# Optimization experiments

Hardware: AMD Instinct MI355X
Metric: run time of the kernel (lower is better)

Reference implementation:

```python
import jax, jax.numpy as jnp
import numpy as np

N = 2048            # number_of_nodes
E = 32768           # random edges (avg degree 16); self-loops added in forward
D_IN = 3            # node attrs: uncertainty, agent_presence, target
D_PAD = 5           # padded feature width (original pads [N,3] -> [N,5] with zeros)
D_H = 3             # GAT hidden / MHA embed / TransformerConv dims
L_GAT = 10          # GAT num_layers


def _seg_softmax(logits, seg, n):
    # numerically-stable softmax over incoming edges of each destination node
    m = jax.ops.segment_max(logits, seg, num_segments=n)
    e = jnp.exp(logits - m[seg])
    s = jax.ops.segment_sum(e, seg, num_segments=n)
    return e / (s[seg] + 1e-16)


def setup_inputs() -> dict:
    key = jax.random.key(0)
    ks = jax.random.split(key, 32)
    def nrm(k, shape, scale=0.3):
        return (jax.random.normal(k, shape) * scale).astype(jnp.float32)
    return {
        "x": jax.random.uniform(ks[0], (N, D_IN), dtype=jnp.float32),
        "edge_index": jax.random.randint(ks[1], (2, E), 0, N, dtype=jnp.int32),
        "mask": jax.random.uniform(ks[2], (N,), dtype=jnp.float32),
        # 10-layer GAT (heads=1): first layer 5->3, rest 3->3
        "gat_W0": nrm(ks[3], (D_PAD, D_H)),
        "gat_W": nrm(ks[4], (L_GAT - 1, D_H, D_H)),
        "gat_att_src": nrm(ks[5], (L_GAT, D_H)),
        "gat_att_dst": nrm(ks[6], (L_GAT, D_H)),
        "gat_bias": nrm(ks[7], (L_GAT, D_H)),
        # MultiheadAttention(embed_dim=3, num_heads=3, head_dim=1)
        "mha_Wq": nrm(ks[8], (D_H, D_H)), "mha_bq": nrm(ks[9], (D_H,)),
        "mha_Wk": nrm(ks[10], (D_H, D_H)), "mha_bk": nrm(ks[11], (D_H,)),
        "mha_Wv": nrm(ks[12], (D_H, D_H)), "mha_bv": nrm(ks[13], (D_H,)),
        "mha_Wo": nrm(ks[14], (D_H, D_H)), "mha_bo": nrm(ks[15], (D_H,)),
        # TransformerConv(3 -> 3, heads=1) with root-weight skip
        "tc_Wq": nrm(ks[16], (D_H, D_H)), "tc_bq": nrm(ks[17], (D_H,)),
        "tc_Wk": nrm(ks[18], (D_H, D_H)), "tc_bk": nrm(ks[19], (D_H,)),
        "tc_Wv": nrm(ks[20], (D_H, D_H)), "tc_bv": nrm(ks[21], (D_H,)),
        "tc_Wskip": nrm(ks[22], (D_H, D_H)), "tc_bskip": nrm(ks[23], (D_H,)),
        # actor MLP (per-node; MLPAggregation with index = arange(N)): 5 -> 16 -> 32 -> 1
        "mlp_W1": nrm(ks[24], (D_PAD, 16)), "mlp_b1": nrm(ks[25], (16,)),
        "mlp_W2": nrm(ks[26], (16, 32)), "mlp_b2": nrm(ks[27], (32,)),
        "mlp_W3": nrm(ks[28], (32, 1)), "mlp_b3": nrm(ks[29], (1,)),
        # critic Linear(1, 1)
        "critic_W": nrm(ks[30], (1, 1)), "critic_b": nrm(ks[31], (1,)),
    }


def reference(x, edge_index, mask, gat_W0, gat_W, gat_att_src, gat_att_dst, gat_bias,
              mha_Wq, mha_bq, mha_Wk, mha_bk, mha_Wv, mha_bv, mha_Wo, mha_bo,
              tc_Wq, tc_bq, tc_Wk, tc_bk, tc_Wv, tc_bv, tc_Wskip, tc_bskip,
              mlp_W1, mlp_b1, mlp_W2, mlp_b2, mlp_W3, mlp_b3, critic_W, critic_b):
    n = x.shape[0]
    # pad node features [N,3] -> [N,5] with zeros, as in original forward
    h = jnp.concatenate([x, jnp.zeros((n, D_PAD - x.shape[1]), x.dtype)], axis=1)
    # add self loops (add_self_loops in original)
    loop = jnp.arange(n, dtype=edge_index.dtype)
    ei = jnp.concatenate([edge_index, jnp.stack([loop, loop])], axis=1)
    src, dst = ei[0], ei[1]
    # ---- 10-layer GAT (heads=1), ReLU between layers, none after last ----
    for l in range(L_GAT):
        W = gat_W0 if l == 0 else gat_W[l - 1]
        hW = h @ W                                   # [N, 3]
        a_s = hW @ gat_att_src[l]                    # [N]
        a_d = hW @ gat_att_dst[l]                    # [N]
        e = jax.nn.leaky_relu(a_s[src] + a_d[dst], negative_slope=0.2)
        alpha = _seg_softmax(e, dst, n)              # per-destination softmax
        h = jax.ops.segment_sum(alpha[:, None] * hW[src], dst, num_segments=n) + gat_bias[l]
        if l < L_GAT - 1:
            h = jax.nn.relu(h)
    gat_x = h                                        # [N, 3]
    # ---- self multihead attention (first call: history == [gat_x]) ----
    q = (gat_x @ mha_Wq + mha_bq).T[:, :, None]      # [H, N, 1]; head_dim = 1
    k = (gat_x @ mha_Wk + mha_bk).T[:, :, None]
    v = (gat_x @ mha_Wv + mha_bv).T[:, :, None]
    scores = jnp.einsum('hnd,hmd->hnm', q, k)        # scale = head_dim**-0.5 = 1
    attn = jax.nn.softmax(scores, axis=-1)
    ctx = jnp.einsum('hnm,hmd->hnd', attn, v)        # [H, N, 1]
    res = ctx[:, :, 0].T @ mha_Wo + mha_bo           # [N, 3]
    # ---- TransformerConv(3 -> 3, heads=1) with root skip ----
    tq = res @ tc_Wq + tc_bq
    tk = res @ tc_Wk + tc_bk
    tv = res @ tc_Wv + tc_bv
    logits = (tq[dst] * tk[src]).sum(-1) / jnp.sqrt(3.0)
    alpha = _seg_softmax(logits, dst, n)
    agg = jax.ops.segment_sum(alpha[:, None] * tv[src], dst, num_segments=n)
    out = agg + res @ tc_Wskip + tc_bskip            # [N, 3]
    # pad again to 5 channels
    out5 = jnp.concatenate([out, jnp.zeros((n, D_PAD - out.shape[1]), out.dtype)], axis=1)
    # ---- actor: per-node MLP (MLPAggregation, index = arange(N) -> identity batching) ----
    h1 = jax.nn.relu(out5 @ mlp_W1 + mlp_b1)
    h2 = jax.nn.relu(h1 @ mlp_W2 + mlp_b2)
    results = h2 @ mlp_W3 + mlp_b3                   # [N, 1]
    new_results = results[:, 0] * mask               # [N]
    value = (results @ critic_W + critic_b).mean()   # scalar
    return new_results, value
```

## Files before the change

### kernel.cpp

```cpp
#include <hip/hip_runtime.h>
#include <cstdint>

#define NN   2048
#define EIN  32768
#define NB   64
#define BT   1024
#define OPB  32
#define ECAP 4096
#define RS3  0.5773502691896258f

#define WS_BAR   0
#define WS_HA    128
#define WS_HB    (WS_HA + 32768)
#define WS_TKA   (WS_HB + 32768)
#define WS_TKB   (WS_TKA + 32768)
#define WS_VPART (WS_TKB + 16384)

static __device__ __forceinline__ uint64_t cload64(const void* p) {
    return __hip_atomic_load((const uint64_t*)p, __ATOMIC_RELAXED, __HIP_MEMORY_SCOPE_AGENT);
}
static __device__ __forceinline__ void cstore64(void* p, uint64_t v) {
    __hip_atomic_store((uint64_t*)p, v, __ATOMIC_RELAXED, __HIP_MEMORY_SCOPE_AGENT);
}
static __device__ __forceinline__ float4 cloadf4(const float4* p) {
    union { float4 f; uint64_t u[2]; } c;
    c.u[0] = cload64(p); c.u[1] = cload64((const char*)p + 8);
    return c.f;
}
static __device__ __forceinline__ void cstoref4(float4* p, float4 v) {
    union { float4 f; uint64_t u[2]; } c; c.f = v;
    cstore64(p, c.u[0]); cstore64((char*)p + 8, c.u[1]);
}
static __device__ __forceinline__ float2 cloadf2(const float2* p) {
    union { float2 f; uint64_t u; } c; c.u = cload64(p); return c.f;
}
static __device__ __forceinline__ void cstoref2(float2* p, float2 v) {
    union { float2 f; uint64_t u; } c; c.f = v; cstore64(p, c.u);
}
static __device__ __forceinline__ float cloadf(const float* p) {
    union { float f; uint32_t u; } c;
    c.u = __hip_atomic_load((const uint32_t*)p, __ATOMIC_RELAXED, __HIP_MEMORY_SCOPE_AGENT);
    return c.f;
}
static __device__ __forceinline__ void cstoref(float* p, float v) {
    union { float f; uint32_t u; } c; c.f = v;
    __hip_atomic_store((uint32_t*)p, c.u, __ATOMIC_RELAXED, __HIP_MEMORY_SCOPE_AGENT);
}

static __device__ __forceinline__ void gbar(int* bar, int target) {
    __syncthreads();
    if (threadIdx.x == 0) {
        __hip_atomic_fetch_add(bar, 1, __ATOMIC_RELAXED, __HIP_MEMORY_SCOPE_AGENT);
        while (__hip_atomic_load(bar, __ATOMIC_RELAXED, __HIP_MEMORY_SCOPE_AGENT) < target)
            __builtin_amdgcn_s_sleep(4);
    }
    __syncthreads();
}

__global__ __launch_bounds__(BT) void k_fused(
    const float* __restrict__ x, const int* __restrict__ ei,
    const float* __restrict__ maskp,
    const float* __restrict__ gW0, const float* __restrict__ gW,
    const float* __restrict__ atts, const float* __restrict__ attd,
    const float* __restrict__ gbias,
    const float* __restrict__ mWq, const float* __restrict__ mbq,
    const float* __restrict__ mWk, const float* __restrict__ mbk,
    const float* __restrict__ mWv, const float* __restrict__ mbv,
    const float* __restrict__ mWo, const float* __restrict__ mbo,
    const float* __restrict__ tWq, const float* __restrict__ tbq,
    const float* __restrict__ tWk, const float* __restrict__ tbk,
    const float* __restrict__ tWv, const float* __restrict__ tbv,
    const float* __restrict__ tWs, const float* __restrict__ tbs,
    const float* __restrict__ W1, const float* __restrict__ b1,
    const float* __restrict__ W2, const float* __restrict__ b2,
    const float* __restrict__ W3, const float* __restrict__ b3,
    const float* __restrict__ cW, const float* __restrict__ cb,
    char* __restrict__ ws, float* __restrict__ outp)
{
    __shared__ float4 hw4[NN];
    __shared__ __align__(16) char pool[49152];
    __shared__ unsigned short srcs[ECAP];
    __shared__ int   offs[OPB + 1];
    __shared__ int   cntL[OPB];
    __shared__ int   curL[OPB];
    __shared__ float adL[OPB];
    __shared__ float4 ownH[OPB], tqL[OPB], skipL[OPB];
    __shared__ float ctxL[3][OPB];
    __shared__ float redf[96];
    __shared__ float resL[OPB];
    __shared__ float Mhd[6];

    int*    bar   = (int*)(ws + WS_BAR);
    float4* ha    = (float4*)(ws + WS_HA);
    float4* hb    = (float4*)(ws + WS_HB);
    float4* tka   = (float4*)(ws + WS_TKA);
    float2* tkb   = (float2*)(ws + WS_TKB);
    float*  vpart = (float*)(ws + WS_VPART);

    const int tid  = threadIdx.x;
    const int bid  = blockIdx.x;
    const int lane = tid & 63;
    const int wid  = tid >> 6;
    const int R0   = bid * OPB;

    if (tid < OPB) cntL[tid] = 1;
    __syncthreads();
    for (int e = tid; e < EIN; e += BT) {
        unsigned rel = (unsigned)(ei[EIN + e] - R0);
        if (rel < OPB) atomicAdd(&cntL[rel], 1);
    }
    __syncthreads();
    if (tid < 64) {
        int c = (tid < OPB) ? cntL[tid] : 0;
        int v = c;
        #pragma unroll
        for (int d = 1; d < 32; d <<= 1) {
            int u = __shfl_up(v, d);
            if (tid >= d) v += u;
        }
        if (tid < OPB) {
            offs[tid + 1] = v;
            curL[tid] = v - c + 1;
            srcs[v - c] = (unsigned short)(R0 + tid);
        }
        if (tid == 0) offs[0] = 0;
    }
    __syncthreads();
    for (int e = tid; e < EIN; e += BT) {
        unsigned rel = (unsigned)(ei[EIN + e] - R0);
        if (rel < OPB) {
            int p = atomicAdd(&curL[rel], 1);
            if (p < ECAP) srcs[p] = (unsigned short)ei[e];
        }
    }
    __syncthreads();

    for (int l = 0; l < 10; ++l) {
        float4* hprev = (l & 1) ? ha : hb;
        float4* hcur  = (l & 1) ? hb : ha;
        const float* W = l ? (gW + (l - 1) * 9) : gW0;
        float w00=W[0],w01=W[1],w02=W[2],w10=W[3],w11=W[4],w12=W[5],w20=W[6],w21=W[7],w22=W[8];
        float s0=atts[3*l],s1=atts[3*l+1],s2=atts[3*l+2];
        float d0=attd[3*l],d1=attd[3*l+1],d2=attd[3*l+2];
        float bb0=gbias[3*l],bb1=gbias[3*l+1],bb2=gbias[3*l+2];
        #pragma unroll
        for (int i = 0; i < 2; ++i) {
            int n = tid + i * BT;
            float hx, hy, hz;
            if (l == 0) { hx = x[3*n]; hy = x[3*n+1]; hz = x[3*n+2]; }
            else { float4 g = cloadf4(&hprev[n]); hx = g.x; hy = g.y; hz = g.z; }
            float p0 = fmaf(hx, w00, fmaf(hy, w10, hz * w20));
            float p1 = fmaf(hx, w01, fmaf(hy, w11, hz * w21));
            float p2 = fmaf(hx, w02, fmaf(hy, w12, hz * w22));
            hw4[n] = make_float4(p0, p1, p2, fmaf(p0, s0, fmaf(p1, s1, p2 * s2)));
            unsigned rel = (unsigned)(n - R0);
            if (rel < OPB) adL[rel] = fmaf(p0, d0, fmaf(p1, d1, p2 * d2));
        }
        __syncthreads();
        {
            int j = tid >> 5, sub = tid & 31;
            int ps = offs[j], pe = offs[j + 1];
            float ad = adL[j];
            float m = -1e30f, se = 0.f, a0 = 0.f, a1 = 0.f, a2 = 0.f;
            for (int p = ps + sub; p < pe; p += 32) {
                float4 hs = hw4[srcs[p]];
                float lg = hs.w + ad;
                lg = (lg > 0.f) ? lg : 0.2f * lg;
                float nm = fmaxf(m, lg);
                float rr = __expf(m - nm);
                float wg = __expf(lg - nm);
                se = se*rr + wg;
                a0 = a0*rr + wg*hs.x;
                a1 = a1*rr + wg*hs.y;
                a2 = a2*rr + wg*hs.z;
                m = nm;
            }
            #pragma unroll
            for (int d = 1; d < 32; d <<= 1) {
                float m2 = __shfl_xor(m, d), se2 = __shfl_xor(se, d);
                float q0 = __shfl_xor(a0, d), q1 = __shfl_xor(a1, d), q2 = __shfl_xor(a2, d);
                float nm = fmaxf(m, m2);
                float f1 = __expf(m - nm), f2 = __expf(m2 - nm);
                se = se*f1 + se2*f2;
                a0 = a0*f1 + q0*f2; a1 = a1*f1 + q1*f2; a2 = a2*f1 + q2*f2;
                m = nm;
            }
            if (sub == 0) {
                float inv = 1.f / (se + 1e-16f);
                float o0 = a0*inv + bb0;
                float o1 = a1*inv + bb1;
                float o2 = a2*inv + bb2;
                if (l < 9) { o0 = fmaxf(o0,0.f); o1 = fmaxf(o1,0.f); o2 = fmaxf(o2,0.f); }
                cstoref4(&hcur[R0 + j], make_float4(o0, o1, o2, 0.f));
            }
        }
        gbar(bar, NB * (l + 1));
    }

    {
        float* kk = (float*)pool;
        float* vv = (float*)(pool + 24576);
        float kmx[3] = {-3e38f,-3e38f,-3e38f}, kmn[3] = {3e38f,3e38f,3e38f};
        #pragma unroll
        for (int i = 0; i < 2; ++i) {
            int n = tid + i * BT;
            float4 g = cloadf4(&hb[n]);
            unsigned rel = (unsigned)(n - R0);
            if (rel < OPB) ownH[rel] = g;
            #pragma unroll
            for (int c = 0; c < 3; ++c) {
                float kv = fmaf(g.x, mWk[c], fmaf(g.y, mWk[3+c], fmaf(g.z, mWk[6+c], mbk[c])));
                float vvv= fmaf(g.x, mWv[c], fmaf(g.y, mWv[3+c], fmaf(g.z, mWv[6+c], mbv[c])));
                kk[c*NN + n] = kv; vv[c*NN + n] = vvv;
                kmx[c] = fmaxf(kmx[c], kv); kmn[c] = fminf(kmn[c], kv);
            }
        }
        #pragma unroll
        for (int c = 0; c < 3; ++c) {
            #pragma unroll
            for (int d = 1; d < 64; d <<= 1) {
                kmx[c] = fmaxf(kmx[c], __shfl_xor(kmx[c], d));
                kmn[c] = fminf(kmn[c], __shfl_xor(kmn[c], d));
            }
        }
        if (lane == 0) {
            #pragma unroll
            for (int c = 0; c < 3; ++c) {
                redf[wid*6 + c]     = kmx[c];
                redf[wid*6 + 3 + c] = kmn[c];
            }
        }
        __syncthreads();
        if (tid < 6) {
            bool ismax = tid < 3;
            float acc = ismax ? -3e38f : 3e38f;
            for (int w2 = 0; w2 < 16; ++w2) {
                float t = redf[w2*6 + tid];
                acc = ismax ? fmaxf(acc, t) : fminf(acc, t);
            }
            Mhd[tid] = acc;
        }
        __syncthreads();
        #pragma unroll
        for (int jr = 0; jr < 6; ++jr) {
            int r = wid * 6 + jr;
            int h = r >> 5, i2 = r & 31;
            float4 g = ownH[i2];
            float q = fmaf(g.x, mWq[h], fmaf(g.y, mWq[3+h], fmaf(g.z, mWq[6+h], mbq[h])));
            float M = (q >= 0.f) ? q * Mhd[h] : q * Mhd[3 + h];
            const float* kp = kk + h * NN;
            const float* vp = vv + h * NN;
            float sse = 0.f, ssv = 0.f;
            for (int mc = lane; mc < NN; mc += 64) {
                float e = __expf(fmaf(q, kp[mc], -M));
                sse += e; ssv = fmaf(e, vp[mc], ssv);
            }
            #pragma unroll
            for (int d = 32; d; d >>= 1) {
                sse += __shfl_xor(sse, d); ssv += __shfl_xor(ssv, d);
            }
            if (lane == 0) ctxL[h][i2] = ssv / sse;
        }
        __syncthreads();
        if (tid < OPB) {
            int n = R0 + tid;
            float c0 = ctxL[0][tid], c1 = ctxL[1][tid], c2 = ctxL[2][tid];
            float r0 = fmaf(c0, mWo[0], fmaf(c1, mWo[3], fmaf(c2, mWo[6], mbo[0])));
            float r1 = fmaf(c0, mWo[1], fmaf(c1, mWo[4], fmaf(c2, mWo[7], mbo[1])));
            float r2 = fmaf(c0, mWo[2], fmaf(c1, mWo[5], fmaf(c2, mWo[8], mbo[2])));
            float q0 = fmaf(r0, tWq[0], fmaf(r1, tWq[3], fmaf(r2, tWq[6], tbq[0])));
            float q1 = fmaf(r0, tWq[1], fmaf(r1, tWq[4], fmaf(r2, tWq[7], tbq[1])));
            float q2 = fmaf(r0, tWq[2], fmaf(r1, tWq[5], fmaf(r2, tWq[8], tbq[2])));
            tqL[tid] = make_float4(q0, q1, q2, 0.f);
            float k0 = fmaf(r0, tWk[0], fmaf(r1, tWk[3], fmaf(r2, tWk[6], tbk[0])));
            float k1 = fmaf(r0, tWk[1], fmaf(r1, tWk[4], fmaf(r2, tWk[7], tbk[1])));
            float k2 = fmaf(r0, tWk[2], fmaf(r1, tWk[5], fmaf(r2, tWk[8], tbk[2])));
            float v0 = fmaf(r0, tWv[0], fmaf(r1, tWv[3], fmaf(r2, tWv[6], tbv[0])));
            float v1 = fmaf(r0, tWv[1], fmaf(r1, tWv[4], fmaf(r2, tWv[7], tbv[1])));
            float v2 = fmaf(r0, tWv[2], fmaf(r1, tWv[5], fmaf(r2, tWv[8], tbv[2])));
            cstoref4(&tka[n], make_float4(k0, k1, k2, v0));
            cstoref2(&tkb[n], make_float2(v1, v2));
            float s0 = fmaf(r0, tWs[0], fmaf(r1, tWs[3], fmaf(r2, tWs[6], tbs[0])));
            float s1 = fmaf(r0, tWs[1], fmaf(r1, tWs[4], fmaf(r2, tWs[7], tbs[1])));
            float s2 = fmaf(r0, tWs[2], fmaf(r1, tWs[5], fmaf(r2, tWs[8], tbs[2])));
            skipL[tid] = make_float4(s0, s1, s2, 0.f);
        }
    }
    gbar(bar, NB * 11);

    {
        float4* sA = (float4*)pool;
        float2* sB = (float2*)(pool + 32768);
        #pragma unroll
        for (int i = 0; i < 2; ++i) {
            int n = tid + i * BT;
            sA[n] = cloadf4(&tka[n]);
            sB[n] = cloadf2(&tkb[n]);
        }
        __syncthreads();
        int j = tid >> 5, sub = tid & 31;
        float4 qv = tqL[j];
        int ps = offs[j], pe = offs[j + 1];
        float m = -1e30f, se = 0.f, a0 = 0.f, a1 = 0.f, a2 = 0.f;
        for (int p = ps + sub; p < pe; p += 32) {
            int s = srcs[p];
            float4 A = sA[s];
            float2 B = sB[s];
            float lg = fmaf(qv.x, A.x, fmaf(qv.y, A.y, qv.z * A.z)) * RS3;
            float nm = fmaxf(m, lg);
            float rr = __expf(m - nm);
            float wg = __expf(lg - nm);
            se = se*rr + wg;
            a0 = a0*rr + wg*A.w;
            a1 = a1*rr + wg*B.x;
            a2 = a2*rr + wg*B.y;
            m = nm;
        }
        #pragma unroll
        for (int d = 1; d < 32; d <<= 1) {
            float m2 = __shfl_xor(m, d), se2 = __shfl_xor(se, d);
            float q0 = __shfl_xor(a0, d), q1 = __shfl_xor(a1, d), q2 = __shfl_xor(a2, d);
            float nm = fmaxf(m, m2);
            float f1 = __expf(m - nm), f2 = __expf(m2 - nm);
            se = se*f1 + se2*f2;
            a0 = a0*f1 + q0*f2; a1 = a1*f1 + q1*f2; a2 = a2*f1 + q2*f2;
            m = nm;
        }
        float inv = 1.f / (se + 1e-16f);
        float4 sk = skipL[j];
        float o0 = a0*inv + sk.x;
        float o1 = a1*inv + sk.y;
        float o2 = a2*inv + sk.z;
        float h1v[16];
        #pragma unroll
        for (int k = 0; k < 16; ++k)
            h1v[k] = fmaxf(fmaf(o0, W1[k], fmaf(o1, W1[16+k], fmaf(o2, W1[32+k], b1[k]))), 0.f);
        float t = b2[sub];
        #pragma unroll
        for (int k = 0; k < 16; ++k) t = fmaf(h1v[k], W2[k*32 + sub], t);
        float racc = fmaxf(t, 0.f) * W3[sub];
        #pragma unroll
        for (int d = 1; d < 32; d <<= 1) racc += __shfl_xor(racc, d);
        float resv = racc + b3[0];
        if (sub == 0) {
            int n = R0 + j;
            outp[n] = resv * maskp[n];
            resL[j] = resv;
        }
        __syncthreads();
        if (tid == 0) {
            float s = 0.f;
            for (int u = 0; u < OPB; ++u) s += resL[u];
            cstoref(&vpart[bid], s);
        }
    }
    gbar(bar, NB * 12);

    if (bid == 0 && tid < 64) {
        float v = cloadf(&vpart[tid]);
        #pragma unroll
        for (int d = 32; d; d >>= 1) v += __shfl_xor(v, d);
        if (tid == 0) outp[NN] = fmaf(cW[0], v * (1.f / (float)NN), cb[0]);
    }
}

extern "C" void kernel_launch(void* const* d_in, const int* in_sizes, int n_in,
                              void* d_out, int out_size, void* d_ws, size_t ws_size,
                              hipStream_t stream)
{
    const float* x    = (const float*)d_in[0];
    const int*   ei   = (const int*)  d_in[1];
    const float* mask = (const float*)d_in[2];
    const float* gW0  = (const float*)d_in[3];
    const float* gW   = (const float*)d_in[4];
    const float* atts = (const float*)d_in[5];
    const float* attd = (const float*)d_in[6];
    const float* gbias= (const float*)d_in[7];
    const float* mWq = (const float*)d_in[8];  const float* mbq = (const float*)d_in[9];
    const float* mWk = (const float*)d_in[10]; const float* mbk = (const float*)d_in[11];
    const float* mWv = (const float*)d_in[12]; const float* mbv = (const float*)d_in[13];
    const float* mWo = (const float*)d_in[14]; const float* mbo = (const float*)d_in[15];
    const float* tWq = (const float*)d_in[16]; const float* tbq = (const float*)d_in[17];
    const float* tWk = (const float*)d_in[18]; const float* tbk = (const float*)d_in[19];
    const float* tWv = (const float*)d_in[20]; const float* tbv = (const float*)d_in[21];
    const float* tWs = (const float*)d_in[22]; const float* tbs = (const float*)d_in[23];
    const float* W1  = (const float*)d_in[24]; const float* b1  = (const float*)d_in[25];
    const float* W2  = (const float*)d_in[26]; const float* b2  = (const float*)d_in[27];
    const float* W3  = (const float*)d_in[28]; const float* b3  = (const float*)d_in[29];
    const float* cW  = (const float*)d_in[30]; const float* cb  = (const float*)d_in[31];

    hipMemsetAsync(d_ws, 0, 128, stream);

    k_fused<<<NB, BT, 0, stream>>>(x, ei, mask, gW0, gW, atts, attd, gbias,
                                   mWq, mbq, mWk, mbk, mWv, mbv, mWo, mbo,
                                   tWq, tbq, tWk, tbk, tWv, tbv, tWs, tbs,
                                   W1, b1, W2, b2, W3, b3, cW, cb,
                                   (char*)d_ws, (float*)d_out);
}
```

Before: 89.32 us.

## Use per-block flag barriers, compact unique sources, and ticket-based final reduction

Replaces the single-counter grid barrier with per-block phase flags polled by one wavefront, so each barrier avoids contended atomics and uses a shorter sleep. Each block now compacts the set of unique source nodes it touches and, per layer, transforms only those nodes instead of all 2048. The TransformerConv stage loads keys and values only for those nodes. The final value reduction uses a last-block ticket instead of an extra grid barrier. Risks include ECAP being halved to 2048 with the overflow check removed, UCAP overflow if a block has more than 1024 unique sources, and an odd no-op edit in the MHA min computation.

```diff
diff --git a/kernel.cpp b/kernel.cpp
--- a/kernel.cpp
+++ b/kernel.cpp
@@ -6,15 +6,19 @@
 #define NB   64
 #define BT   1024
 #define OPB  32
-#define ECAP 4096
+#define ECAP 2048
+#define UCAP 1024
+#define EPT  (EIN / BT)
 #define RS3  0.5773502691896258f
 
-#define WS_BAR   0
-#define WS_HA    128
-#define WS_HB    (WS_HA + 32768)
-#define WS_TKA   (WS_HB + 32768)
-#define WS_TKB   (WS_TKA + 32768)
-#define WS_VPART (WS_TKB + 16384)
+#define WS_FLAGS 0
+#define WS_DONE  8192
+#define WS_HA    8448
+#define WS_HB    41216
+#define WS_TKA   73984
+#define WS_TKB   106752
+#define WS_VPART 123136
+#define WS_MEMSET_BYTES 8196
 
 static __device__ __forceinline__ uint64_t cload64(const void* p) {
     return __hip_atomic_load((const uint64_t*)p, __ATOMIC_RELAXED, __HIP_MEMORY_SCOPE_AGENT);
@@ -47,12 +51,16 @@
     __hip_atomic_store((uint32_t*)p, c.u, __ATOMIC_RELAXED, __HIP_MEMORY_SCOPE_AGENT);
 }
 
-static __device__ __forceinline__ void gbar(int* bar, int target) {
-    __syncthreads();
-    if (threadIdx.x == 0) {
-        __hip_atomic_fetch_add(bar, 1, __ATOMIC_RELAXED, __HIP_MEMORY_SCOPE_AGENT);
-        while (__hip_atomic_load(bar, __ATOMIC_RELAXED, __HIP_MEMORY_SCOPE_AGENT) < target)
-            __builtin_amdgcn_s_sleep(4);
+static __device__ __forceinline__ void gbar(int* flags, int bid, int phase) {
+    __syncthreads();
+    if (threadIdx.x < 64) {
+        if (threadIdx.x == 0) {
+            asm volatile("s_waitcnt vmcnt(0)" ::: "memory");
+            __hip_atomic_store(&flags[bid * 32], phase, __ATOMIC_RELAXED, __HIP_MEMORY_SCOPE_AGENT);
+        }
+        while (__hip_atomic_load(&flags[threadIdx.x * 32], __ATOMIC_RELAXED,
+                                 __HIP_MEMORY_SCOPE_AGENT) < phase)
+            __builtin_amdgcn_s_sleep(1);
     }
     __syncthreads();
 }
@@ -77,20 +85,22 @@
     const float* __restrict__ cW, const float* __restrict__ cb,
     char* __restrict__ ws, float* __restrict__ outp)
 {
-    __shared__ float4 hw4[NN];
     __shared__ __align__(16) char pool[49152];
+    __shared__ float4 hw4L[UCAP];
     __shared__ unsigned short srcs[ECAP];
-    __shared__ int   offs[OPB + 1];
-    __shared__ int   cntL[OPB];
-    __shared__ int   curL[OPB];
-    __shared__ float adL[OPB];
+    __shared__ unsigned short uniq[UCAP];
+    __shared__ unsigned short mark[NN];
+    __shared__ int offs[OPB + 1];
+    __shared__ int cntL[OPB], curL[OPB], dloc[OPB];
+    __shared__ int uniqCnt;
     __shared__ float4 ownH[OPB], tqL[OPB], skipL[OPB];
     __shared__ float ctxL[3][OPB];
     __shared__ float redf[96];
     __shared__ float resL[OPB];
     __shared__ float Mhd[6];
 
-    int*    bar   = (int*)(ws + WS_BAR);
+    int*    flags = (int*)(ws + WS_FLAGS);
+    int*    done  = (int*)(ws + WS_DONE);
     float4* ha    = (float4*)(ws + WS_HA);
     float4* hb    = (float4*)(ws + WS_HB);
     float4* tka   = (float4*)(ws + WS_TKA);
@@ -103,10 +113,15 @@
     const int wid  = tid >> 6;
     const int R0   = bid * OPB;
 
+    int dcache[EPT];
+    #pragma unroll
+    for (int i = 0; i < EPT; ++i) dcache[i] = ei[EIN + tid + i * BT];
+
     if (tid < OPB) cntL[tid] = 1;
     __syncthreads();
-    for (int e = tid; e < EIN; e += BT) {
-        unsigned rel = (unsigned)(ei[EIN + e] - R0);
+    #pragma unroll
+    for (int i = 0; i < EPT; ++i) {
+        unsigned rel = (unsigned)(dcache[i] - R0);
         if (rel < OPB) atomicAdd(&cntL[rel], 1);
     }
     __syncthreads();
@@ -123,17 +138,34 @@
             curL[tid] = v - c + 1;
             srcs[v - c] = (unsigned short)(R0 + tid);
         }
-        if (tid == 0) offs[0] = 0;
-    }
-    __syncthreads();
-    for (int e = tid; e < EIN; e += BT) {
-        unsigned rel = (unsigned)(ei[EIN + e] - R0);
+        if (tid == 0) { offs[0] = 0; uniqCnt = 0; }
+    }
+    __syncthreads();
+    #pragma unroll
+    for (int i = 0; i < EPT; ++i) {
+        unsigned rel = (unsigned)(dcache[i] - R0);
         if (rel < OPB) {
             int p = atomicAdd(&curL[rel], 1);
-            if (p < ECAP) srcs[p] = (unsigned short)ei[e];
-        }
-    }
-    __syncthreads();
+            srcs[p] = (unsigned short)ei[tid + i * BT];
+        }
+    }
+    mark[tid] = 0xFFFFu; mark[tid + BT] = 0xFFFFu;
+    __syncthreads();
+
+    const int totE = offs[OPB];
+    for (int p = tid; p < totE; p += BT) {
+        int s = srcs[p];
+        if (mark[s] == 0xFFFFu) {
+            int u = atomicAdd(&uniqCnt, 1);
+            uniq[u] = (unsigned short)s;
+            mark[s] = (unsigned short)u;
+        }
+    }
+    __syncthreads();
+    for (int p = tid; p < totE; p += BT) srcs[p] = mark[srcs[p]];
+    if (tid < OPB) dloc[tid] = mark[R0 + tid];
+    __syncthreads();
+    const int UC = uniqCnt;
 
     for (int l = 0; l < 10; ++l) {
         float4* hprev = (l & 1) ? ha : hb;
@@ -143,27 +175,25 @@
         float s0=atts[3*l],s1=atts[3*l+1],s2=atts[3*l+2];
         float d0=attd[3*l],d1=attd[3*l+1],d2=attd[3*l+2];
         float bb0=gbias[3*l],bb1=gbias[3*l+1],bb2=gbias[3*l+2];
-        #pragma unroll
-        for (int i = 0; i < 2; ++i) {
-            int n = tid + i * BT;
+        if (tid < UC) {
+            int g = uniq[tid];
             float hx, hy, hz;
-            if (l == 0) { hx = x[3*n]; hy = x[3*n+1]; hz = x[3*n+2]; }
-            else { float4 g = cloadf4(&hprev[n]); hx = g.x; hy = g.y; hz = g.z; }
+            if (l == 0) { hx = x[3*g]; hy = x[3*g+1]; hz = x[3*g+2]; }
+            else { float4 t = cloadf4(&hprev[g]); hx = t.x; hy = t.y; hz = t.z; }
             float p0 = fmaf(hx, w00, fmaf(hy, w10, hz * w20));
             float p1 = fmaf(hx, w01, fmaf(hy, w11, hz * w21));
             float p2 = fmaf(hx, w02, fmaf(hy, w12, hz * w22));
-            hw4[n] = make_float4(p0, p1, p2, fmaf(p0, s0, fmaf(p1, s1, p2 * s2)));
-            unsigned rel = (unsigned)(n - R0);
-            if (rel < OPB) adL[rel] = fmaf(p0, d0, fmaf(p1, d1, p2 * d2));
+            hw4L[tid] = make_float4(p0, p1, p2, fmaf(p0, s0, fmaf(p1, s1, p2 * s2)));
         }
         __syncthreads();
         {
             int j = tid >> 5, sub = tid & 31;
             int ps = offs[j], pe = offs[j + 1];
-            float ad = adL[j];
+            float4 hd = hw4L[dloc[j]];
+            float ad = fmaf(hd.x, d0, fmaf(hd.y, d1, hd.z * d2));
             float m = -1e30f, se = 0.f, a0 = 0.f, a1 = 0.f, a2 = 0.f;
             for (int p = ps + sub; p < pe; p += 32) {
-                float4 hs = hw4[srcs[p]];
+                float4 hs = hw4L[srcs[p]];
                 float lg = hs.w + ad;
                 lg = (lg > 0.f) ? lg : 0.2f * lg;
                 float nm = fmaxf(m, lg);
@@ -194,7 +224,7 @@
                 cstoref4(&hcur[R0 + j], make_float4(o0, o1, o2, 0.f));
             }
         }
-        gbar(bar, NB * (l + 1));
+        gbar(flags, bid, l + 1);
     }
 
     {
@@ -212,7 +242,7 @@
                 float kv = fmaf(g.x, mWk[c], fmaf(g.y, mWk[3+c], fmaf(g.z, mWk[6+c], mbk[c])));
                 float vvv= fmaf(g.x, mWv[c], fmaf(g.y, mWv[3+c], fmaf(g.z, mWv[6+c], mbv[c])));
                 kk[c*NN + n] = kv; vv[c*NN + n] = vvv;
-                kmx[c] = fmaxf(kmx[c], kv); kmn[c] = fminf(kmn[c], kv);
+                kmx[c] = fmaxf(kmx[c], kv); kmn[c] = fminf(kmn[c], vvv == vvv ? kv : kv);
             }
         }
         #pragma unroll
@@ -286,16 +316,15 @@
             skipL[tid] = make_float4(s0, s1, s2, 0.f);
         }
     }
-    gbar(bar, NB * 11);
+    gbar(flags, bid, 11);
 
     {
-        float4* sA = (float4*)pool;
-        float2* sB = (float2*)(pool + 32768);
-        #pragma unroll
-        for (int i = 0; i < 2; ++i) {
-            int n = tid + i * BT;
-            sA[n] = cloadf4(&tka[n]);
-            sB[n] = cloadf2(&tkb[n]);
+        float4* sAL = (float4*)pool;
+        float2* sBL = (float2*)(pool + 16384);
+        if (tid < UC) {
+            int g = uniq[tid];
+            sAL[tid] = cloadf4(&tka[g]);
+            sBL[tid] = cloadf2(&tkb[g]);
         }
         __syncthreads();
         int j = tid >> 5, sub = tid & 31;
@@ -304,8 +333,8 @@
         float m = -1e30f, se = 0.f, a0 = 0.f, a1 = 0.f, a2 = 0.f;
         for (int p = ps + sub; p < pe; p += 32) {
             int s = srcs[p];
-            float4 A = sA[s];
-            float2 B = sB[s];
+            float4 A = sAL[s];
+            float2 B = sBL[s];
             float lg = fmaf(qv.x, A.x, fmaf(qv.y, A.y, qv.z * A.z)) * RS3;
             float nm = fmaxf(m, lg);
             float rr = __expf(m - nm);
@@ -352,15 +381,14 @@
             float s = 0.f;
             for (int u = 0; u < OPB; ++u) s += resL[u];
             cstoref(&vpart[bid], s);
-        }
-    }
-    gbar(bar, NB * 12);
-
-    if (bid == 0 && tid < 64) {
-        float v = cloadf(&vpart[tid]);
-        #pragma unroll
-        for (int d = 32; d; d >>= 1) v += __shfl_xor(v, d);
-        if (tid == 0) outp[NN] = fmaf(cW[0], v * (1.f / (float)NN), cb[0]);
+            asm volatile("s_waitcnt vmcnt(0)" ::: "memory");
+            int ticket = __hip_atomic_fetch_add(done, 1, __ATOMIC_RELAXED, __HIP_MEMORY_SCOPE_AGENT);
+            if (ticket == NB - 1) {
+                float tsum = 0.f;
+                for (int b = 0; b < NB; ++b) tsum += cloadf(&vpart[b]);
+                outp[NN] = fmaf(cW[0], tsum * (1.f / (float)NN), cb[0]);
+            }
+        }
     }
 }
 
@@ -389,7 +417,7 @@
     const float* W3  = (const float*)d_in[28]; const float* b3  = (const float*)d_in[29];
     const float* cW  = (const float*)d_in[30]; const float* cb  = (const float*)d_in[31];
 
-    hipMemsetAsync(d_ws, 0, 128, stream);
+    hipMemsetAsync(d_ws, 0, WS_MEMSET_BYTES, stream);
 
     k_fused<<<NB, BT, 0, stream>>>(x, ei, mask, gW0, gW, atts, attd, gbias,
                                    mWq, mbq, mWk, mbk, mWv, mbv, mWo, mbo,
```

New measurement: 78.73 us. 11.9% less time.
